# Kernel optimization log

Hardware: AMD Instinct MI355X
Metric: run time of the kernel (lower is better)

The kernel has to match this reference:

```python
import jax, jax.numpy as jnp
import numpy as np
from jax import lax

# Per-tensor power-of-two scales (ScalingImplType.CONST / POWER_OF_TWO in Brevitas)
S_ACT8 = 2.0 ** -4   # 8-bit signed input quant scale
S_ACT4 = 2.0 ** -1   # 4-bit signed input quant scale
S_W = 2.0 ** -2      # per-tensor weight quant scale
S_RELU = 2.0 ** -2   # 4-bit unsigned QuantReLU scale


def fq(x, scale, qmin, qmax):
    # fake-quant with straight-through estimator (STE)
    q = jnp.clip(jnp.round(x / scale), qmin, qmax) * scale
    return x + lax.stop_gradient(q - x)


def fq_signed(x, scale, bits):
    return fq(x, scale, -(2 ** (bits - 1)), 2 ** (bits - 1) - 1)


def fq_uint(x, scale, bits):
    return fq(x, scale, 0, 2 ** bits - 1)


def qconv(x, w, in_bits, w_bits, s_in, stride=1, padding=0, groups=1):
    xq = fq_signed(x, s_in, in_bits)
    wq = fq_signed(w, S_W, w_bits)
    return lax.conv_general_dilated(
        xq, wq, (stride, stride), [(padding, padding)] * 2,
        feature_group_count=groups,
        dimension_numbers=('NCHW', 'OIHW', 'NCHW'))


def maxpool(x, k, s):
    return lax.reduce_window(x, -jnp.inf, lax.max,
                             (1, 1, k, k), (1, 1, s, s), 'VALID')


def dwsep(x, dw, pw):
    c = x.shape[1]
    x = qconv(x, dw, 4, 4, S_ACT4, padding=1, groups=c)  # depthwise 3x3
    x = qconv(x, pw, 4, 4, S_ACT4)                       # pointwise 1x1
    return x


def qrelu4(x):
    return fq_uint(jax.nn.relu(x), S_RELU, 4)


def setup_inputs() -> dict:
    key = jax.random.key(0)
    ks = jax.random.split(key, 10)
    B = 1024
    mk = lambda k, shp, sc=0.5: jax.random.normal(k, shp, jnp.float32) * sc
    return {
        'x': jax.random.normal(ks[0], (B, 3, 32, 32), jnp.float32),
        'w0': mk(ks[1], (3, 3, 1, 1)),
        'dw1': mk(ks[2], (3, 1, 3, 3)),
        'pw1': mk(ks[3], (32, 3, 1, 1)),
        'dw2': mk(ks[4], (32, 1, 3, 3)),
        'pw2': mk(ks[5], (64, 32, 1, 1)),
        'dw3': mk(ks[6], (64, 1, 3, 3)),
        'pw3': mk(ks[7], (128, 64, 1, 1)),
        'wc1': mk(ks[8], (256, 128, 1, 1)),
        'wc2': mk(ks[9], (10, 256, 1, 1)),
    }


def reference(x, w0, dw1, pw1, dw2, pw2, dw3, pw3, wc1, wc2):
    # features
    h = qconv(x, w0, 8, 8, S_ACT8)            # 1x1, 3->3, 8-bit
    h = dwsep(h, dw1, pw1)                    # 3->32, 32x32
    h = qrelu4(h)
    h = maxpool(h, 2, 2)                      # 16x16
    h = dwsep(h, dw2, pw2)                    # 32->64
    h = qrelu4(h)
    h = maxpool(h, 2, 2)                      # 8x8
    h = dwsep(h, dw3, pw3)                    # 64->128
    h = qrelu4(h)
    h = maxpool(h, 8, 1)                      # 1x1
    # classifier
    h = qconv(h, wc1, 4, 4, S_ACT4)           # 128->256
    h = qrelu4(h)
    h = qconv(h, wc2, 4, 4, S_ACT4)           # 256->10
    h = fq_signed(h, S_ACT8, 8)               # output quant int8
    return h
```

## Files before the change

kernel.cpp:

```cpp
#include <hip/hip_runtime.h>

typedef int v4i __attribute__((ext_vector_type(4)));

#define W0i   0
#define DW1i  9
#define PW1i  36
#define DW2i  132
#define WC1p  3556
#define WC2p  11748
#define PW2Fb 12388
#define PW3Fb 12900
#define DW2pk 14948
#define DW3pk 15092
#define WTOT  15380

__device__ __attribute__((aligned(16))) int g_wsq[WTOT];

__device__ __forceinline__ int iclamp(int v, int lo, int hi) {
  return v < lo ? lo : (v > hi ? hi : v);
}
__device__ __forceinline__ int rne4(int a) {
  return (a + 1 + ((a >> 2) & 1)) >> 2;
}
__device__ __forceinline__ int rne32(int a) {
  return (a + 15 + ((a >> 5) & 1)) >> 5;
}

__device__ __forceinline__ void bar_lds() {
  asm volatile("s_waitcnt lgkmcnt(0)\n\ts_barrier" ::: "memory");
}

__device__ __forceinline__ int dot4(int a, int b, int c) {
#if defined(__has_builtin) && __has_builtin(__builtin_amdgcn_sdot4)
  return __builtin_amdgcn_sdot4(a, b, c, false);
#else
  c += ((a << 24) >> 24) * ((b << 24) >> 24);
  c += ((a << 16) >> 24) * ((b << 16) >> 24);
  c += ((a <<  8) >> 24) * ((b <<  8) >> 24);
  c += (a >> 24) * (b >> 24);
  return c;
#endif
}

__device__ __forceinline__ int alignb(int hi, int lo, int sh) {
#if defined(__has_builtin) && __has_builtin(__builtin_amdgcn_alignbyte)
  return __builtin_amdgcn_alignbyte(hi, lo, sh);
#else
  return (int)(((((unsigned long long)(unsigned)hi) << 32) |
                (unsigned)lo) >> (8 * sh));
#endif
}

__device__ __forceinline__ int pack3(int a, int b, int c) {
  return (a & 0xff) | ((b & 0xff) << 8) | ((c & 0xff) << 16);
}

__device__ __forceinline__ int pk_mad16(int a, int b, int c) {
  int d;
  asm("v_pk_mad_i16 %0, %1, %2, %3" : "=v"(d) : "v"(a), "v"(b), "v"(c));
  return d;
}
__device__ __forceinline__ int pk_add16(int a, int b) {
  int d;
  asm("v_pk_add_i16 %0, %1, %2" : "=v"(d) : "v"(a), "v"(b));
  return d;
}
__device__ __forceinline__ int pk_ashr16(int sh, int a) {
  int d;
  asm("v_pk_ashrrev_i16 %0, %1, %2" : "=v"(d) : "v"(sh), "v"(a));
  return d;
}
__device__ __forceinline__ int pk_max16(int a, int b) {
  int d;
  asm("v_pk_max_i16 %0, %1, %2" : "=v"(d) : "v"(a), "v"(b));
  return d;
}
__device__ __forceinline__ int pk_min16(int a, int b) {
  int d;
  asm("v_pk_min_i16 %0, %1, %2" : "=v"(d) : "v"(a), "v"(b));
  return d;
}
__device__ __forceinline__ int rne4s_pk(int a) {
  const int sh = 0x00020002, one = 0x00010001;
  int t = pk_ashr16(sh, a);
  t &= one;
  t += one;
  int s4 = pk_add16(a, t);
  int r = pk_ashr16(sh, s4);
  r = pk_max16(r, (int)0xFFF8FFF8);
  r = pk_min16(r, 0x00070007);
  return r;
}

__device__ __forceinline__ int max4(v4i d) {
  int a = d[0] > d[1] ? d[0] : d[1];
  int b = d[2] > d[3] ? d[2] : d[3];
  return a > b ? a : b;
}

__global__ __launch_bounds__(256) void prep_weights(
    const float* __restrict__ w0,  const float* __restrict__ dw1,
    const float* __restrict__ pw1, const float* __restrict__ dw2,
    const float* __restrict__ pw2, const float* __restrict__ dw3,
    const float* __restrict__ pw3, const float* __restrict__ wc1,
    const float* __restrict__ wc2) {
  int t = blockIdx.x * blockDim.x + threadIdx.x;
  if (t >= WTOT) return;
  if (t >= DW2i && t < WC1p) return;
  if (t < DW2i) {
    float w; int lo = -8, hi = 7;
    if (t < DW1i)      { w = w0[t];        lo = -128; hi = 127; }
    else if (t < PW1i)   w = dw1[t - DW1i];
    else                 w = pw1[t - PW1i];
    g_wsq[t] = iclamp((int)rintf(w * 4.f), lo, hi);
  } else if (t < PW2Fb) {
    const float* src = (t < WC2p) ? wc1 + (t - WC1p) * 4
                                  : wc2 + (t - WC2p) * 4;
    int p = 0;
#pragma unroll
    for (int b = 0; b < 4; b++) {
      int c = iclamp((int)rintf(src[b] * 4.f), -8, 7);
      p |= (c & 0xff) << (8 * b);
    }
    g_wsq[t] = p;
  } else if (t < DW2pk) {
    int i = t - PW2Fb;
    int nt = i >> 7, r = i & 127, lane = r >> 1, dw = r & 1;
    int n = nt * 16 + (lane & 15);
    int kb = (lane >> 4) * 8 + dw * 4;
    int p = 0;
#pragma unroll
    for (int b = 0; b < 4; b++) {
      int c = iclamp((int)rintf(pw2[n * 32 + kb + b] * 4.f), -8, 7);
      p |= (c & 0xff) << (8 * b);
    }
    g_wsq[t] = p;
  } else if (t < DW2pk + 144) {
    int i = t - DW2pk;
    int cq = i / 18, r = i - cq * 18, t9 = r >> 1, par = r & 1;
    int wl = iclamp((int)rintf(dw2[(cq * 4 + par) * 9 + t9] * 4.f), -8, 7);
    int wh = iclamp((int)rintf(dw2[(cq * 4 + 2 + par) * 9 + t9] * 4.f), -8, 7);
    g_wsq[t] = (wl & 0xFFFF) | (wh << 16);
  } else {
    int i = t - DW3pk;
    int cq = i / 18, r = i - cq * 18, t9 = r >> 1, par = r & 1;
    int wl = iclamp((int)rintf(dw3[(cq * 4 + par) * 9 + t9] * 4.f), -8, 7);
    int wh = iclamp((int)rintf(dw3[(cq * 4 + 2 + par) * 9 + t9] * 4.f), -8, 7);
    g_wsq[t] = (wl & 0xFFFF) | (wh << 16);
  }
}

__global__ __launch_bounds__(256) void prep_weights_pw3(
    const float* __restrict__ pw3) {
  int t = PW3Fb + blockIdx.x * blockDim.x + threadIdx.x;
  if (t >= DW2pk) return;
  int i = t - PW3Fb;
  int g = i >> 7, r = i & 127, lane = r >> 1, dw = r & 1;
  int nt = g >> 1, kh = g & 1;
  int n = nt * 16 + (lane & 15);
  int kb = kh * 32 + (lane >> 4) * 8 + dw * 4;
  int p = 0;
#pragma unroll
  for (int b = 0; b < 4; b++) {
    int c = iclamp((int)rintf(pw3[n * 64 + kb + b] * 4.f), -8, 7);
    p |= (c & 0xff) << (8 * b);
  }
  g_wsq[t] = p;
}

__global__ __launch_bounds__(256, 4) void fused_net(
    const float* __restrict__ x,
    float* __restrict__ out)
{
  const int img = blockIdx.x;
  const int tid = threadIdx.x;
  const int wv = tid >> 6, lane = tid & 63;
  const int lm = lane & 15, kg = lane >> 4;
  const int* __restrict__ wq = g_wsq;

  __shared__ __align__(16) int bufAi[2560];
  __shared__ __align__(16) int bufBi[2592];

  const int ntp = (wv & 1) * 2;
  const long bw0 = *(const long*)(wq + PW2Fb + (ntp * 64 + lane) * 2);
  const long bw1 = *(const long*)(wq + PW2Fb + ((ntp + 1) * 64 + lane) * 2);
  long b0v[2], b1v[2];
#pragma unroll
  for (int h = 0; h < 2; h++) {
    int nt = wv * 2 + h;
    b0v[h] = *(const long*)(wq + PW3Fb + (nt * 2 + 0) * 128 + lane * 2);
    b1v[h] = *(const long*)(wq + PW3Fb + (nt * 2 + 1) * 128 + lane * 2);
  }

  {
    const float* xim = x + (size_t)img * 3072;
    const int p4 = tid * 4;
    float4 v0 = *(const float4*)(xim + p4);
    float4 v1 = *(const float4*)(xim + 1024 + p4);
    float4 v2 = *(const float4*)(xim + 2048 + p4);
    int w[9];
#pragma unroll
    for (int i = 0; i < 9; i++) w[i] = wq[W0i + i];
#define Q8(v) iclamp((int)rintf((v) * 16.f), -128, 127)
    int a0[4] = {Q8(v0.x), Q8(v0.y), Q8(v0.z), Q8(v0.w)};
    int a1[4] = {Q8(v1.x), Q8(v1.y), Q8(v1.z), Q8(v1.w)};
    int a2[4] = {Q8(v2.x), Q8(v2.y), Q8(v2.z), Q8(v2.w)};
#undef Q8
#pragma unroll
    for (int o = 0; o < 3; o++) {
      int pk = 0;
#pragma unroll
      for (int j = 0; j < 4; j++) {
        int s = a0[j] * w[o * 3] + a1[j] * w[o * 3 + 1] + a2[j] * w[o * 3 + 2];
        pk |= (iclamp(rne32(s), -8, 7) & 0xff) << (8 * j);
      }
      bufAi[o * 256 + tid] = pk;
    }
  }
  bar_lds();

  {
    const int py = tid >> 4, px = tid & 15;
    int wr[3][3], wrh[3][3];
#pragma unroll
    for (int c = 0; c < 3; c++)
#pragma unroll
      for (int ky = 0; ky < 3; ky++) {
        int w = pack3(wq[DW1i + c * 9 + ky * 3],
                      wq[DW1i + c * 9 + ky * 3 + 1],
                      wq[DW1i + c * 9 + ky * 3 + 2]);
        wr[c][ky] = w;
        wrh[c][ky] = w << 8;
      }
    const int s = (px & 1) ? 1 : 3;
    const int D0 = (2 * px - 1) >> 2;
    int V[3][4];
#pragma unroll
    for (int r = 0; r < 4; r++) {
      int rr = 2 * py - 1 + r;
      bool ok = (unsigned)rr < 32u;
#pragma unroll
      for (int c = 0; c < 3; c++) {
        int lo = 0, hi = 0;
        if (ok) {
          const int* ap = bufAi + c * 256 + rr * 8;
          if (px > 0)  lo = ap[D0];
          if (px < 15) hi = ap[D0 + 1];
        }
        V[c][r] = alignb(hi, lo, s);
      }
    }
    int a[4];
#pragma unroll
    for (int dy = 0; dy < 2; dy++) {
      int r01[3];
#pragma unroll
      for (int c = 0; c < 3; c++) {
        int acc0 = 0, acc1 = 0;
#pragma unroll
        for (int ky = 0; ky < 3; ky++) {
          acc0 = dot4(V[c][dy + ky], wr[c][ky], acc0);
          acc1 = dot4(V[c][dy + ky], wrh[c][ky], acc1);
        }
        int p = (int)__builtin_amdgcn_perm((unsigned)acc1, (unsigned)acc0,
                                           0x05040100u);
        r01[c] = rne4s_pk(p);
      }
      unsigned t0 = __builtin_amdgcn_perm((unsigned)r01[1], (unsigned)r01[0],
                                          0x0C0C0400u);
      a[2 * dy] = (int)__builtin_amdgcn_perm((unsigned)r01[2], t0, 0x0C040100u);
      unsigned t1 = __builtin_amdgcn_perm((unsigned)r01[1], (unsigned)r01[0],
                                          0x0C0C0602u);
      a[2 * dy + 1] =
          (int)__builtin_amdgcn_perm((unsigned)r01[2], t1, 0x0C060100u);
    }
#pragma unroll
    for (int it = 0; it < 8; it++) {
      int pk = 0;
#pragma unroll
      for (int j = 0; j < 4; j++) {
        int o = it * 4 + j;
        int wpk = pack3(wq[PW1i + o * 3], wq[PW1i + o * 3 + 1],
                        wq[PW1i + o * 3 + 2]);
        int m0 = dot4(a[0], wpk, 0), m1 = dot4(a[1], wpk, 0);
        int m2 = dot4(a[2], wpk, 0), m3 = dot4(a[3], wpk, 0);
        int mx = max(max(m0, m1), max(m2, m3));
        pk |= iclamp(rne4(mx), 0, 7) << (8 * j);
      }
      bufBi[py * 149 + px * 9 + it] = pk;
    }
  }
  bar_lds();

  {
    const int cq = tid >> 5;
    const int rem = tid & 31;
    const int y = rem >> 1, xh = rem & 1, x0 = xh * 8;
    int we[9], wo[9];
    {
      const int2* wp = (const int2*)(wq + DW2pk + cq * 18);
#pragma unroll
      for (int t9 = 0; t9 < 9; t9++) { int2 v = wp[t9]; we[t9] = v.x; wo[t9] = v.y; }
    }
    int acce[8] = {}, acco[8] = {};
#pragma unroll
    for (int ky = 0; ky < 3; ky++) {
      int yy = y + ky - 1;
      if (yy < 0 || yy > 15) continue;
      int rb = yy * 149 + cq;
      int rd[10];
      rd[0] = (x0 > 0) ? bufBi[rb + (x0 - 1) * 9] : 0;
#pragma unroll
      for (int k = 1; k < 9; k++) rd[k] = bufBi[rb + (x0 - 1 + k) * 9];
      rd[9] = (x0 < 8) ? bufBi[rb + (x0 + 8) * 9] : 0;
      int ee[10], eo[10];
#pragma unroll
      for (int k = 0; k < 10; k++) {
        ee[k] = rd[k] & 0x000F000F;
        eo[k] = (rd[k] >> 8) & 0x000F000F;
      }
#pragma unroll
      for (int j = 0; j < 8; j++)
#pragma unroll
        for (int kx = 0; kx < 3; kx++) {
          acce[j] = pk_mad16(ee[j + kx], we[ky * 3 + kx], acce[j]);
          acco[j] = pk_mad16(eo[j + kx], wo[ky * 3 + kx], acco[j]);
        }
    }
    const int py = y >> 1, dy = y & 1;
#pragma unroll
    for (int j = 0; j < 8; j++) {
      int xx = x0 + j;
      int qp = py * 8 + (xx >> 1);
      int q = qp ^ (py & 3);
      int m = q * 4 + dy * 2 + (xx & 1);
      int re = rne4s_pk(acce[j]);
      int ro = rne4s_pk(acco[j]);
      bufAi[m * 10 + cq] = (re & 0x00FF00FF) | ((ro & 0x00FF00FF) << 8);
    }
  }
  bar_lds();

  {
    const int mtb = (wv >> 1) * 8;
    const signed char* Ab = (const signed char*)bufAi;
    signed char* A2c = (signed char*)bufBi;
    const int n0 = ntp * 16 + lm, n1 = (ntp + 1) * 16 + lm;
#pragma unroll 4
    for (int mt = mtb; mt < mtb + 8; mt++) {
      int m = mt * 16 + lm;
      long av = *(const long*)(Ab + m * 40 + kg * 8);
      v4i d0 = __builtin_amdgcn_mfma_i32_16x16x32_i8(av, bw0, (v4i){0, 0, 0, 0},
                                                     0, 0, 0);
      v4i d1 = __builtin_amdgcn_mfma_i32_16x16x32_i8(av, bw1, (v4i){0, 0, 0, 0},
                                                     0, 0, 0);
      int q = mt * 4 + kg;
      int qp = q ^ ((q >> 3) & 3);
      int py = qp >> 3, px = qp & 7;
      int bb = (py * 137 + px * 17) * 4;
      A2c[bb + n0] = (signed char)iclamp(rne4(max4(d0)), 0, 7);
      A2c[bb + n1] = (signed char)iclamp(rne4(max4(d1)), 0, 7);
    }
  }
  bar_lds();

  {
    int cq2 = tid >> 4;
    int s = tid & 15;
    int y = s >> 1, x0 = (s & 1) << 2;
    int we[9], wo[9];
    {
      const int2* wp = (const int2*)(wq + DW3pk + cq2 * 18);
#pragma unroll
      for (int t9 = 0; t9 < 9; t9++) { int2 v = wp[t9]; we[t9] = v.x; wo[t9] = v.y; }
    }
    int acce[4] = {}, acco[4] = {};
#pragma unroll
    for (int ky = 0; ky < 3; ky++) {
      int yy = y + ky - 1;
      if (yy < 0 || yy > 7) continue;
      int rb = yy * 137 + cq2;
      int rd[6];
      rd[0] = (x0 == 4) ? bufBi[rb + (x0 - 1) * 17] : 0;
      rd[1] = bufBi[rb + x0 * 17];
      rd[2] = bufBi[rb + (x0 + 1) * 17];
      rd[3] = bufBi[rb + (x0 + 2) * 17];
      rd[4] = bufBi[rb + (x0 + 3) * 17];
      rd[5] = (x0 == 0) ? bufBi[rb + (x0 + 4) * 17] : 0;
      int ee[6], eo[6];
#pragma unroll
      for (int k = 0; k < 6; k++) {
        ee[k] = rd[k] & 0x000F000F;
        eo[k] = (rd[k] >> 8) & 0x000F000F;
      }
#pragma unroll
      for (int j = 0; j < 4; j++)
#pragma unroll
        for (int kx = 0; kx < 3; kx++) {
          acce[j] = pk_mad16(ee[j + kx], we[ky * 3 + kx], acce[j]);
          acco[j] = pk_mad16(eo[j + kx], wo[ky * 3 + kx], acco[j]);
        }
    }
#pragma unroll
    for (int j = 0; j < 4; j++) {
      int re = rne4s_pk(acce[j]);
      int ro = rne4s_pk(acco[j]);
      bufAi[(y * 8 + x0 + j) * 18 + cq2] =
          (re & 0x00FF00FF) | ((ro & 0x00FF00FF) << 8);
    }
  }
  int4 wfc[8];
  {
    const int4* wp = (const int4*)(wq + WC1p + tid * 32);
#pragma unroll
    for (int rI = 0; rI < 8; rI++) wfc[rI] = wp[rI];
  }
  bar_lds();

  {
    const signed char* Ab = (const signed char*)bufAi;
    signed char* fcin = (signed char*)bufBi;
    int mx[2] = {-1000000, -1000000};
#pragma unroll
    for (int mt = 0; mt < 4; mt++) {
      int m = mt * 16 + lm;
      long a0 = *(const long*)(Ab + m * 72 + kg * 8);
      long a1 = *(const long*)(Ab + m * 72 + 32 + kg * 8);
#pragma unroll
      for (int h = 0; h < 2; h++) {
        v4i d = __builtin_amdgcn_mfma_i32_16x16x32_i8(a0, b0v[h],
                                                      (v4i){0, 0, 0, 0}, 0, 0, 0);
        d = __builtin_amdgcn_mfma_i32_16x16x32_i8(a1, b1v[h], d, 0, 0, 0);
        int t4 = max4(d);
        mx[h] = mx[h] > t4 ? mx[h] : t4;
      }
    }
#pragma unroll
    for (int h = 0; h < 2; h++) {
      int red = max(mx[h], __shfl_xor(mx[h], 16));
      red = max(red, __shfl_xor(red, 32));
      if (lane < 16)
        fcin[(wv * 2 + h) * 16 + lm] = (signed char)iclamp(rne4(red), 0, 7);
    }
  }
  bar_lds();

  {
    const int4* mp = (const int4*)bufBi;
    int acc = 0;
#pragma unroll
    for (int rI = 0; rI < 8; rI++) {
      int4 a = mp[rI]; int4 w = wfc[rI];
      acc = dot4(a.x, w.x, acc); acc = dot4(a.y, w.y, acc);
      acc = dot4(a.z, w.z, acc); acc = dot4(a.w, w.w, acc);
    }
    ((signed char*)bufAi)[tid] = (signed char)iclamp(rne4(acc), 0, 7);
  }
  bar_lds();

  if (tid < 40) {
    int k = tid >> 2, j = tid & 3;
    const int4* wp = (const int4*)(wq + WC2p + k * 64 + j * 16);
    const int4* ap = (const int4*)bufAi;
    int acc = 0;
#pragma unroll
    for (int r = 0; r < 4; r++) {
      int4 a = ap[j * 4 + r]; int4 w = wp[r];
      acc = dot4(a.x, w.x, acc); acc = dot4(a.y, w.y, acc);
      acc = dot4(a.z, w.z, acc); acc = dot4(a.w, w.w, acc);
    }
    acc += __shfl_xor(acc, 1);
    acc += __shfl_xor(acc, 2);
    if (j == 0) {
      int code = iclamp(2 * acc, -128, 127);
      out[(size_t)img * 10 + k] = (float)code * 0.0625f;
    }
  }
}

extern "C" void kernel_launch(void* const* d_in, const int* in_sizes, int n_in,
                              void* d_out, int out_size, void* d_ws, size_t ws_size,
                              hipStream_t stream) {
  (void)d_ws; (void)ws_size; (void)in_sizes; (void)n_in; (void)out_size;
  const float* x   = (const float*)d_in[0];
  const float* w0  = (const float*)d_in[1];
  const float* dw1 = (const float*)d_in[2];
  const float* pw1 = (const float*)d_in[3];
  const float* dw2 = (const float*)d_in[4];
  const float* pw2 = (const float*)d_in[5];
  const float* dw3 = (const float*)d_in[6];
  const float* pw3 = (const float*)d_in[7];
  const float* wc1 = (const float*)d_in[8];
  const float* wc2 = (const float*)d_in[9];
  float* out = (float*)d_out;

  prep_weights<<<(WTOT + 255) / 256, 256, 0, stream>>>(
      w0, dw1, pw1, dw2, pw2, dw3, pw3, wc1, wc2);
  prep_weights_pw3<<<(DW2pk - PW3Fb + 255) / 256, 256, 0, stream>>>(pw3);
  fused_net<<<1024, 256, 0, stream>>>(x, out);
}
```

Before: 98.83 us.

## Process two images per block and fold pw3 weight prep into main prep kernel

Each block now handles two images with doubled LDS buffers, amortizing per-block weight register loads and barrier overhead over twice the work; grid halves to 512 blocks and launch bounds drop to 2 blocks/CU. The pw1 pointwise weights are hoisted into 32 registers once, and the separate pw3 weight-prep kernel is merged into the main prep kernel, removing one launch. This risks lower occupancy and fewer blocks than CUs (512 blocks on a 256-CU device gives two per CU), plus higher register pressure.

Result: faster. 96.72 us (-2.1%).

```diff
diff --git a/kernel.cpp b/kernel.cpp
--- a/kernel.cpp
+++ b/kernel.cpp
@@ -123,7 +123,7 @@
       p |= (c & 0xff) << (8 * b);
     }
     g_wsq[t] = p;
-  } else if (t < DW2pk) {
+  } else if (t < PW3Fb) {
     int i = t - PW2Fb;
     int nt = i >> 7, r = i & 127, lane = r >> 1, dw = r & 1;
     int n = nt * 16 + (lane & 15);
@@ -135,7 +135,20 @@
       p |= (c & 0xff) << (8 * b);
     }
     g_wsq[t] = p;
-  } else if (t < DW2pk + 144) {
+  } else if (t < DW2pk) {
+    int i = t - PW3Fb;
+    int g = i >> 7, r = i & 127, lane = r >> 1, dw = r & 1;
+    int nt = g >> 1, kh = g & 1;
+    int n = nt * 16 + (lane & 15);
+    int kb = kh * 32 + (lane >> 4) * 8 + dw * 4;
+    int p = 0;
+#pragma unroll
+    for (int b = 0; b < 4; b++) {
+      int c = iclamp((int)rintf(pw3[n * 64 + kb + b] * 4.f), -8, 7);
+      p |= (c & 0xff) << (8 * b);
+    }
+    g_wsq[t] = p;
+  } else if (t < DW3pk) {
     int i = t - DW2pk;
     int cq = i / 18, r = i - cq * 18, t9 = r >> 1, par = r & 1;
     int wl = iclamp((int)rintf(dw2[(cq * 4 + par) * 9 + t9] * 4.f), -8, 7);
@@ -150,36 +163,18 @@
   }
 }
 
-__global__ __launch_bounds__(256) void prep_weights_pw3(
-    const float* __restrict__ pw3) {
-  int t = PW3Fb + blockIdx.x * blockDim.x + threadIdx.x;
-  if (t >= DW2pk) return;
-  int i = t - PW3Fb;
-  int g = i >> 7, r = i & 127, lane = r >> 1, dw = r & 1;
-  int nt = g >> 1, kh = g & 1;
-  int n = nt * 16 + (lane & 15);
-  int kb = kh * 32 + (lane >> 4) * 8 + dw * 4;
-  int p = 0;
-#pragma unroll
-  for (int b = 0; b < 4; b++) {
-    int c = iclamp((int)rintf(pw3[n * 64 + kb + b] * 4.f), -8, 7);
-    p |= (c & 0xff) << (8 * b);
-  }
-  g_wsq[t] = p;
-}
-
-__global__ __launch_bounds__(256, 4) void fused_net(
+__global__ __launch_bounds__(256, 2) void fused_net(
     const float* __restrict__ x,
     float* __restrict__ out)
 {
-  const int img = blockIdx.x;
+  const int img0 = blockIdx.x * 2;
   const int tid = threadIdx.x;
   const int wv = tid >> 6, lane = tid & 63;
   const int lm = lane & 15, kg = lane >> 4;
   const int* __restrict__ wq = g_wsq;
 
-  __shared__ __align__(16) int bufAi[2560];
-  __shared__ __align__(16) int bufBi[2592];
+  __shared__ __align__(16) int bufAi[2][2560];
+  __shared__ __align__(16) int bufBi[2][2592];
 
   const int ntp = (wv & 1) * 2;
   const long bw0 = *(const long*)(wq + PW2Fb + (ntp * 64 + lane) * 2);
@@ -193,29 +188,41 @@
   }
 
   {
-    const float* xim = x + (size_t)img * 3072;
     const int p4 = tid * 4;
-    float4 v0 = *(const float4*)(xim + p4);
-    float4 v1 = *(const float4*)(xim + 1024 + p4);
-    float4 v2 = *(const float4*)(xim + 2048 + p4);
+    float4 v[2][3];
+#pragma unroll
+    for (int ii = 0; ii < 2; ii++) {
+      const float* xim = x + (size_t)(img0 + ii) * 3072;
+      v[ii][0] = *(const float4*)(xim + p4);
+      v[ii][1] = *(const float4*)(xim + 1024 + p4);
+      v[ii][2] = *(const float4*)(xim + 2048 + p4);
+    }
     int w[9];
 #pragma unroll
     for (int i = 0; i < 9; i++) w[i] = wq[W0i + i];
-#define Q8(v) iclamp((int)rintf((v) * 16.f), -128, 127)
-    int a0[4] = {Q8(v0.x), Q8(v0.y), Q8(v0.z), Q8(v0.w)};
-    int a1[4] = {Q8(v1.x), Q8(v1.y), Q8(v1.z), Q8(v1.w)};
-    int a2[4] = {Q8(v2.x), Q8(v2.y), Q8(v2.z), Q8(v2.w)};
+#define Q8(vv) iclamp((int)rintf((vv) * 16.f), -128, 127)
+#pragma unroll
+    for (int ii = 0; ii < 2; ii++) {
+      int aq[3][4];
+#pragma unroll
+      for (int c = 0; c < 3; c++) {
+        float4 vv = v[ii][c];
+        aq[c][0] = Q8(vv.x); aq[c][1] = Q8(vv.y);
+        aq[c][2] = Q8(vv.z); aq[c][3] = Q8(vv.w);
+      }
+#pragma unroll
+      for (int o = 0; o < 3; o++) {
+        int pk = 0;
+#pragma unroll
+        for (int j = 0; j < 4; j++) {
+          int s = aq[0][j] * w[o * 3] + aq[1][j] * w[o * 3 + 1] +
+                  aq[2][j] * w[o * 3 + 2];
+          pk |= (iclamp(rne32(s), -8, 7) & 0xff) << (8 * j);
+        }
+        bufAi[ii][o * 256 + tid] = pk;
+      }
+    }
 #undef Q8
-#pragma unroll
-    for (int o = 0; o < 3; o++) {
-      int pk = 0;
-#pragma unroll
-      for (int j = 0; j < 4; j++) {
-        int s = a0[j] * w[o * 3] + a1[j] * w[o * 3 + 1] + a2[j] * w[o * 3 + 2];
-        pk |= (iclamp(rne32(s), -8, 7) & 0xff) << (8 * j);
-      }
-      bufAi[o * 256 + tid] = pk;
-    }
   }
   bar_lds();
 
@@ -232,62 +239,69 @@
         wr[c][ky] = w;
         wrh[c][ky] = w << 8;
       }
+    int wpw[32];
+#pragma unroll
+    for (int o = 0; o < 32; o++)
+      wpw[o] = pack3(wq[PW1i + o * 3], wq[PW1i + o * 3 + 1],
+                     wq[PW1i + o * 3 + 2]);
     const int s = (px & 1) ? 1 : 3;
     const int D0 = (2 * px - 1) >> 2;
-    int V[3][4];
-#pragma unroll
-    for (int r = 0; r < 4; r++) {
-      int rr = 2 * py - 1 + r;
-      bool ok = (unsigned)rr < 32u;
-#pragma unroll
-      for (int c = 0; c < 3; c++) {
-        int lo = 0, hi = 0;
-        if (ok) {
-          const int* ap = bufAi + c * 256 + rr * 8;
-          if (px > 0)  lo = ap[D0];
-          if (px < 15) hi = ap[D0 + 1];
-        }
-        V[c][r] = alignb(hi, lo, s);
-      }
-    }
-    int a[4];
-#pragma unroll
-    for (int dy = 0; dy < 2; dy++) {
-      int r01[3];
-#pragma unroll
-      for (int c = 0; c < 3; c++) {
-        int acc0 = 0, acc1 = 0;
-#pragma unroll
-        for (int ky = 0; ky < 3; ky++) {
-          acc0 = dot4(V[c][dy + ky], wr[c][ky], acc0);
-          acc1 = dot4(V[c][dy + ky], wrh[c][ky], acc1);
-        }
-        int p = (int)__builtin_amdgcn_perm((unsigned)acc1, (unsigned)acc0,
-                                           0x05040100u);
-        r01[c] = rne4s_pk(p);
-      }
-      unsigned t0 = __builtin_amdgcn_perm((unsigned)r01[1], (unsigned)r01[0],
-                                          0x0C0C0400u);
-      a[2 * dy] = (int)__builtin_amdgcn_perm((unsigned)r01[2], t0, 0x0C040100u);
-      unsigned t1 = __builtin_amdgcn_perm((unsigned)r01[1], (unsigned)r01[0],
-                                          0x0C0C0602u);
-      a[2 * dy + 1] =
-          (int)__builtin_amdgcn_perm((unsigned)r01[2], t1, 0x0C060100u);
-    }
-#pragma unroll
-    for (int it = 0; it < 8; it++) {
-      int pk = 0;
-#pragma unroll
-      for (int j = 0; j < 4; j++) {
-        int o = it * 4 + j;
-        int wpk = pack3(wq[PW1i + o * 3], wq[PW1i + o * 3 + 1],
-                        wq[PW1i + o * 3 + 2]);
-        int m0 = dot4(a[0], wpk, 0), m1 = dot4(a[1], wpk, 0);
-        int m2 = dot4(a[2], wpk, 0), m3 = dot4(a[3], wpk, 0);
-        int mx = max(max(m0, m1), max(m2, m3));
-        pk |= iclamp(rne4(mx), 0, 7) << (8 * j);
-      }
-      bufBi[py * 149 + px * 9 + it] = pk;
+#pragma unroll
+    for (int ii = 0; ii < 2; ii++) {
+      int V[3][4];
+#pragma unroll
+      for (int r = 0; r < 4; r++) {
+        int rr = 2 * py - 1 + r;
+        bool ok = (unsigned)rr < 32u;
+#pragma unroll
+        for (int c = 0; c < 3; c++) {
+          int lo = 0, hi = 0;
+          if (ok) {
+            const int* ap = &bufAi[ii][c * 256 + rr * 8];
+            if (px > 0)  lo = ap[D0];
+            if (px < 15) hi = ap[D0 + 1];
+          }
+          V[c][r] = alignb(hi, lo, s);
+        }
+      }
+      int a[4];
+#pragma unroll
+      for (int dy = 0; dy < 2; dy++) {
+        int r01[3];
+#pragma unroll
+        for (int c = 0; c < 3; c++) {
+          int acc0 = 0, acc1 = 0;
+#pragma unroll
+          for (int ky = 0; ky < 3; ky++) {
+            acc0 = dot4(V[c][dy + ky], wr[c][ky], acc0);
+            acc1 = dot4(V[c][dy + ky], wrh[c][ky], acc1);
+          }
+          int p = (int)__builtin_amdgcn_perm((unsigned)acc1, (unsigned)acc0,
+                                             0x05040100u);
+          r01[c] = rne4s_pk(p);
+        }
+        unsigned t0 = __builtin_amdgcn_perm((unsigned)r01[1], (unsigned)r01[0],
+                                            0x0C0C0400u);
+        a[2 * dy] =
+            (int)__builtin_amdgcn_perm((unsigned)r01[2], t0, 0x0C040100u);
+        unsigned t1 = __builtin_amdgcn_perm((unsigned)r01[1], (unsigned)r01[0],
+                                            0x0C0C0602u);
+        a[2 * dy + 1] =
+            (int)__builtin_amdgcn_perm((unsigned)r01[2], t1, 0x0C060100u);
+      }
+#pragma unroll
+      for (int it = 0; it < 8; it++) {
+        int pk = 0;
+#pragma unroll
+        for (int j = 0; j < 4; j++) {
+          int wpk = wpw[it * 4 + j];
+          int m0 = dot4(a[0], wpk, 0), m1 = dot4(a[1], wpk, 0);
+          int m2 = dot4(a[2], wpk, 0), m3 = dot4(a[3], wpk, 0);
+          int mx = max(max(m0, m1), max(m2, m3));
+          pk |= iclamp(rne4(mx), 0, 7) << (8 * j);
+        }
+        bufBi[ii][py * 149 + px * 9 + it] = pk;
+      }
     }
   }
   bar_lds();
@@ -302,64 +316,70 @@
 #pragma unroll
       for (int t9 = 0; t9 < 9; t9++) { int2 v = wp[t9]; we[t9] = v.x; wo[t9] = v.y; }
     }
-    int acce[8] = {}, acco[8] = {};
-#pragma unroll
-    for (int ky = 0; ky < 3; ky++) {
-      int yy = y + ky - 1;
-      if (yy < 0 || yy > 15) continue;
-      int rb = yy * 149 + cq;
-      int rd[10];
-      rd[0] = (x0 > 0) ? bufBi[rb + (x0 - 1) * 9] : 0;
-#pragma unroll
-      for (int k = 1; k < 9; k++) rd[k] = bufBi[rb + (x0 - 1 + k) * 9];
-      rd[9] = (x0 < 8) ? bufBi[rb + (x0 + 8) * 9] : 0;
-      int ee[10], eo[10];
-#pragma unroll
-      for (int k = 0; k < 10; k++) {
-        ee[k] = rd[k] & 0x000F000F;
-        eo[k] = (rd[k] >> 8) & 0x000F000F;
-      }
-#pragma unroll
-      for (int j = 0; j < 8; j++)
-#pragma unroll
-        for (int kx = 0; kx < 3; kx++) {
-          acce[j] = pk_mad16(ee[j + kx], we[ky * 3 + kx], acce[j]);
-          acco[j] = pk_mad16(eo[j + kx], wo[ky * 3 + kx], acco[j]);
-        }
-    }
     const int py = y >> 1, dy = y & 1;
 #pragma unroll
-    for (int j = 0; j < 8; j++) {
-      int xx = x0 + j;
-      int qp = py * 8 + (xx >> 1);
-      int q = qp ^ (py & 3);
-      int m = q * 4 + dy * 2 + (xx & 1);
-      int re = rne4s_pk(acce[j]);
-      int ro = rne4s_pk(acco[j]);
-      bufAi[m * 10 + cq] = (re & 0x00FF00FF) | ((ro & 0x00FF00FF) << 8);
+    for (int ii = 0; ii < 2; ii++) {
+      int acce[8] = {}, acco[8] = {};
+#pragma unroll
+      for (int ky = 0; ky < 3; ky++) {
+        int yy = y + ky - 1;
+        if (yy < 0 || yy > 15) continue;
+        int rb = yy * 149 + cq;
+        int rd[10];
+        rd[0] = (x0 > 0) ? bufBi[ii][rb + (x0 - 1) * 9] : 0;
+#pragma unroll
+        for (int k = 1; k < 9; k++) rd[k] = bufBi[ii][rb + (x0 - 1 + k) * 9];
+        rd[9] = (x0 < 8) ? bufBi[ii][rb + (x0 + 8) * 9] : 0;
+        int ee[10], eo[10];
+#pragma unroll
+        for (int k = 0; k < 10; k++) {
+          ee[k] = rd[k] & 0x000F000F;
+          eo[k] = (rd[k] >> 8) & 0x000F000F;
+        }
+#pragma unroll
+        for (int j = 0; j < 8; j++)
+#pragma unroll
+          for (int kx = 0; kx < 3; kx++) {
+            acce[j] = pk_mad16(ee[j + kx], we[ky * 3 + kx], acce[j]);
+            acco[j] = pk_mad16(eo[j + kx], wo[ky * 3 + kx], acco[j]);
+          }
+      }
+#pragma unroll
+      for (int j = 0; j < 8; j++) {
+        int xx = x0 + j;
+        int qp = py * 8 + (xx >> 1);
+        int q = qp ^ (py & 3);
+        int m = q * 4 + dy * 2 + (xx & 1);
+        int re = rne4s_pk(acce[j]);
+        int ro = rne4s_pk(acco[j]);
+        bufAi[ii][m * 10 + cq] = (re & 0x00FF00FF) | ((ro & 0x00FF00FF) << 8);
+      }
     }
   }
   bar_lds();
 
   {
     const int mtb = (wv >> 1) * 8;
-    const signed char* Ab = (const signed char*)bufAi;
-    signed char* A2c = (signed char*)bufBi;
     const int n0 = ntp * 16 + lm, n1 = (ntp + 1) * 16 + lm;
+#pragma unroll
+    for (int ii = 0; ii < 2; ii++) {
+      const signed char* Ab = (const signed char*)bufAi[ii];
+      signed char* A2c = (signed char*)bufBi[ii];
 #pragma unroll 4
-    for (int mt = mtb; mt < mtb + 8; mt++) {
-      int m = mt * 16 + lm;
-      long av = *(const long*)(Ab + m * 40 + kg * 8);
-      v4i d0 = __builtin_amdgcn_mfma_i32_16x16x32_i8(av, bw0, (v4i){0, 0, 0, 0},
-                                                     0, 0, 0);
-      v4i d1 = __builtin_amdgcn_mfma_i32_16x16x32_i8(av, bw1, (v4i){0, 0, 0, 0},
-                                                     0, 0, 0);
-      int q = mt * 4 + kg;
-      int qp = q ^ ((q >> 3) & 3);
-      int py = qp >> 3, px = qp & 7;
-      int bb = (py * 137 + px * 17) * 4;
-      A2c[bb + n0] = (signed char)iclamp(rne4(max4(d0)), 0, 7);
-      A2c[bb + n1] = (signed char)iclamp(rne4(max4(d1)), 0, 7);
+      for (int mt = mtb; mt < mtb + 8; mt++) {
+        int m = mt * 16 + lm;
+        long av = *(const long*)(Ab + m * 40 + kg * 8);
+        v4i d0 = __builtin_amdgcn_mfma_i32_16x16x32_i8(av, bw0,
+                                                       (v4i){0, 0, 0, 0}, 0, 0, 0);
+        v4i d1 = __builtin_amdgcn_mfma_i32_16x16x32_i8(av, bw1,
+                                                       (v4i){0, 0, 0, 0}, 0, 0, 0);
+        int q = mt * 4 + kg;
+        int qp = q ^ ((q >> 3) & 3);
+        int py = qp >> 3, px = qp & 7;
+        int bb = (py * 137 + px * 17) * 4;
+        A2c[bb + n0] = (signed char)iclamp(rne4(max4(d0)), 0, 7);
+        A2c[bb + n1] = (signed char)iclamp(rne4(max4(d1)), 0, 7);
+      }
     }
   }
   bar_lds();
@@ -374,39 +394,42 @@
 #pragma unroll
       for (int t9 = 0; t9 < 9; t9++) { int2 v = wp[t9]; we[t9] = v.x; wo[t9] = v.y; }
     }
-    int acce[4] = {}, acco[4] = {};
-#pragma unroll
-    for (int ky = 0; ky < 3; ky++) {
-      int yy = y + ky - 1;
-      if (yy < 0 || yy > 7) continue;
-      int rb = yy * 137 + cq2;
-      int rd[6];
-      rd[0] = (x0 == 4) ? bufBi[rb + (x0 - 1) * 17] : 0;
-      rd[1] = bufBi[rb + x0 * 17];
-      rd[2] = bufBi[rb + (x0 + 1) * 17];
-      rd[3] = bufBi[rb + (x0 + 2) * 17];
-      rd[4] = bufBi[rb + (x0 + 3) * 17];
-      rd[5] = (x0 == 0) ? bufBi[rb + (x0 + 4) * 17] : 0;
-      int ee[6], eo[6];
-#pragma unroll
-      for (int k = 0; k < 6; k++) {
-        ee[k] = rd[k] & 0x000F000F;
-        eo[k] = (rd[k] >> 8) & 0x000F000F;
-      }
-#pragma unroll
-      for (int j = 0; j < 4; j++)
-#pragma unroll
-        for (int kx = 0; kx < 3; kx++) {
-          acce[j] = pk_mad16(ee[j + kx], we[ky * 3 + kx], acce[j]);
-          acco[j] = pk_mad16(eo[j + kx], wo[ky * 3 + kx], acco[j]);
-        }
-    }
-#pragma unroll
-    for (int j = 0; j < 4; j++) {
-      int re = rne4s_pk(acce[j]);
-      int ro = rne4s_pk(acco[j]);
-      bufAi[(y * 8 + x0 + j) * 18 + cq2] =
-          (re & 0x00FF00FF) | ((ro & 0x00FF00FF) << 8);
+#pragma unroll
+    for (int ii = 0; ii < 2; ii++) {
+      int acce[4] = {}, acco[4] = {};
+#pragma unroll
+      for (int ky = 0; ky < 3; ky++) {
+        int yy = y + ky - 1;
+        if (yy < 0 || yy > 7) continue;
+        int rb = yy * 137 + cq2;
+        int rd[6];
+        rd[0] = (x0 == 4) ? bufBi[ii][rb + (x0 - 1) * 17] : 0;
+        rd[1] = bufBi[ii][rb + x0 * 17];
+        rd[2] = bufBi[ii][rb + (x0 + 1) * 17];
+        rd[3] = bufBi[ii][rb + (x0 + 2) * 17];
+        rd[4] = bufBi[ii][rb + (x0 + 3) * 17];
+        rd[5] = (x0 == 0) ? bufBi[ii][rb + (x0 + 4) * 17] : 0;
+        int ee[6], eo[6];
+#pragma unroll
+        for (int k = 0; k < 6; k++) {
+          ee[k] = rd[k] & 0x000F000F;
+          eo[k] = (rd[k] >> 8) & 0x000F000F;
+        }
+#pragma unroll
+        for (int j = 0; j < 4; j++)
+#pragma unroll
+          for (int kx = 0; kx < 3; kx++) {
+            acce[j] = pk_mad16(ee[j + kx], we[ky * 3 + kx], acce[j]);
+            acco[j] = pk_mad16(eo[j + kx], wo[ky * 3 + kx], acco[j]);
+          }
+      }
+#pragma unroll
+      for (int j = 0; j < 4; j++) {
+        int re = rne4s_pk(acce[j]);
+        int ro = rne4s_pk(acco[j]);
+        bufAi[ii][(y * 8 + x0 + j) * 18 + cq2] =
+            (re & 0x00FF00FF) | ((ro & 0x00FF00FF) << 8);
+      }
     }
   }
   int4 wfc[8];
@@ -418,62 +441,72 @@
   bar_lds();
 
   {
-    const signed char* Ab = (const signed char*)bufAi;
-    signed char* fcin = (signed char*)bufBi;
-    int mx[2] = {-1000000, -1000000};
-#pragma unroll
-    for (int mt = 0; mt < 4; mt++) {
-      int m = mt * 16 + lm;
-      long a0 = *(const long*)(Ab + m * 72 + kg * 8);
-      long a1 = *(const long*)(Ab + m * 72 + 32 + kg * 8);
+#pragma unroll
+    for (int ii = 0; ii < 2; ii++) {
+      const signed char* Ab = (const signed char*)bufAi[ii];
+      signed char* fcin = (signed char*)bufBi[ii];
+      int mx[2] = {-1000000, -1000000};
+#pragma unroll
+      for (int mt = 0; mt < 4; mt++) {
+        int m = mt * 16 + lm;
+        long a0 = *(const long*)(Ab + m * 72 + kg * 8);
+        long a1 = *(const long*)(Ab + m * 72 + 32 + kg * 8);
+#pragma unroll
+        for (int h = 0; h < 2; h++) {
+          v4i d = __builtin_amdgcn_mfma_i32_16x16x32_i8(a0, b0v[h],
+                                                        (v4i){0, 0, 0, 0}, 0, 0, 0);
+          d = __builtin_amdgcn_mfma_i32_16x16x32_i8(a1, b1v[h], d, 0, 0, 0);
+          int t4 = max4(d);
+          mx[h] = mx[h] > t4 ? mx[h] : t4;
+        }
+      }
 #pragma unroll
       for (int h = 0; h < 2; h++) {
-        v4i d = __builtin_amdgcn_mfma_i32_16x16x32_i8(a0, b0v[h],
-                                                      (v4i){0, 0, 0, 0}, 0, 0, 0);
-        d = __builtin_amdgcn_mfma_i32_16x16x32_i8(a1, b1v[h], d, 0, 0, 0);
-        int t4 = max4(d);
-        mx[h] = mx[h] > t4 ? mx[h] : t4;
-      }
-    }
-#pragma unroll
-    for (int h = 0; h < 2; h++) {
-      int red = max(mx[h], __shfl_xor(mx[h], 16));
-      red = max(red, __shfl_xor(red, 32));
-      if (lane < 16)
-        fcin[(wv * 2 + h) * 16 + lm] = (signed char)iclamp(rne4(red), 0, 7);
-    }
-  }
-  bar_lds();
-
-  {
-    const int4* mp = (const int4*)bufBi;
-    int acc = 0;
-#pragma unroll
-    for (int rI = 0; rI < 8; rI++) {
-      int4 a = mp[rI]; int4 w = wfc[rI];
-      acc = dot4(a.x, w.x, acc); acc = dot4(a.y, w.y, acc);
-      acc = dot4(a.z, w.z, acc); acc = dot4(a.w, w.w, acc);
-    }
-    ((signed char*)bufAi)[tid] = (signed char)iclamp(rne4(acc), 0, 7);
-  }
-  bar_lds();
-
-  if (tid < 40) {
-    int k = tid >> 2, j = tid & 3;
-    const int4* wp = (const int4*)(wq + WC2p + k * 64 + j * 16);
-    const int4* ap = (const int4*)bufAi;
-    int acc = 0;
-#pragma unroll
-    for (int r = 0; r < 4; r++) {
-      int4 a = ap[j * 4 + r]; int4 w = wp[r];
-      acc = dot4(a.x, w.x, acc); acc = dot4(a.y, w.y, acc);
-      acc = dot4(a.z, w.z, acc); acc = dot4(a.w, w.w, acc);
-    }
-    acc += __shfl_xor(acc, 1);
-    acc += __shfl_xor(acc, 2);
-    if (j == 0) {
-      int code = iclamp(2 * acc, -128, 127);
-      out[(size_t)img * 10 + k] = (float)code * 0.0625f;
+        int red = max(mx[h], __shfl_xor(mx[h], 16));
+        red = max(red, __shfl_xor(red, 32));
+        if (lane < 16)
+          fcin[(wv * 2 + h) * 16 + lm] = (signed char)iclamp(rne4(red), 0, 7);
+      }
+    }
+  }
+  bar_lds();
+
+  {
+#pragma unroll
+    for (int ii = 0; ii < 2; ii++) {
+      const int4* mp = (const int4*)bufBi[ii];
+      int acc = 0;
+#pragma unroll
+      for (int rI = 0; rI < 8; rI++) {
+        int4 a = mp[rI]; int4 w = wfc[rI];
+        acc = dot4(a.x, w.x, acc); acc = dot4(a.y, w.y, acc);
+        acc = dot4(a.z, w.z, acc); acc = dot4(a.w, w.w, acc);
+      }
+      ((signed char*)bufAi[ii])[tid] = (signed char)iclamp(rne4(acc), 0, 7);
+    }
+  }
+  bar_lds();
+
+  {
+    const int half = tid >> 7;
+    const int t = tid & 127;
+    if (t < 40) {
+      int k = t >> 2, j = t & 3;
+      const int4* wp = (const int4*)(wq + WC2p + k * 64 + j * 16);
+      const int4* ap = (const int4*)bufAi[half];
+      int acc = 0;
+#pragma unroll
+      for (int r = 0; r < 4; r++) {
+        int4 a = ap[j * 4 + r]; int4 w = wp[r];
+        acc = dot4(a.x, w.x, acc); acc = dot4(a.y, w.y, acc);
+        acc = dot4(a.z, w.z, acc); acc = dot4(a.w, w.w, acc);
+      }
+      acc += __shfl_xor(acc, 1);
+      acc += __shfl_xor(acc, 2);
+      if (j == 0) {
+        int code = iclamp(2 * acc, -128, 127);
+        out[(size_t)(img0 + half) * 10 + k] = (float)code * 0.0625f;
+      }
     }
   }
 }
@@ -496,6 +529,5 @@
 
   prep_weights<<<(WTOT + 255) / 256, 256, 0, stream>>>(
       w0, dw1, pw1, dw2, pw2, dw3, pw3, wc1, wc2);
-  prep_weights_pw3<<<(DW2pk - PW3Fb + 255) / 256, 256, 0, stream>>>(pw3);
-  fused_net<<<1024, 256, 0, stream>>>(x, out);
-}
+  fused_net<<<512, 256, 0, stream>>>(x, out);
+}
```

## Double fused_net block to 512 threads and merge weight prep into one kernel

Applied to the files above, without the earlier changes.

Each per-image block now runs 512 threads, and every stage is repartitioned so each thread does half the work. This covers the pointwise-1 channel halves, the dw2/dw3 columns, the pw2 m-tiles, the pw3 n-tiles and a split-K FC1 with a shuffle reduction. The pw3 weight prep is folded into the single prep kernel, and pw1/dw1 weights are prepacked to skip per-thread pack3 work. The goal is more parallelism per image and one fewer launch, at the cost of higher register-pressure limits and some stages (the input conv) leaving half the threads idle.

After: 93.45 us. 1.06x faster.

```diff
diff --git a/kernel.cpp b/kernel.cpp
--- a/kernel.cpp
+++ b/kernel.cpp
@@ -6,6 +6,8 @@
 #define DW1i  9
 #define PW1i  36
 #define DW2i  132
+#define PW1pk 132
+#define DW1pk 164
 #define WC1p  3556
 #define WC2p  11748
 #define PW2Fb 12388
@@ -54,6 +56,9 @@
 __device__ __forceinline__ int pack3(int a, int b, int c) {
   return (a & 0xff) | ((b & 0xff) << 8) | ((c & 0xff) << 16);
 }
+__device__ __forceinline__ int q4w(float w) {
+  return iclamp((int)rintf(w * 4.f), -8, 7);
+}
 
 __device__ __forceinline__ int pk_mad16(int a, int b, int c) {
   int d;
@@ -106,13 +111,20 @@
     const float* __restrict__ wc2) {
   int t = blockIdx.x * blockDim.x + threadIdx.x;
   if (t >= WTOT) return;
-  if (t >= DW2i && t < WC1p) return;
   if (t < DW2i) {
     float w; int lo = -8, hi = 7;
     if (t < DW1i)      { w = w0[t];        lo = -128; hi = 127; }
     else if (t < PW1i)   w = dw1[t - DW1i];
     else                 w = pw1[t - PW1i];
     g_wsq[t] = iclamp((int)rintf(w * 4.f), lo, hi);
+  } else if (t < PW1pk + 32) {
+    int o = t - PW1pk;
+    g_wsq[t] = pack3(q4w(pw1[3 * o]), q4w(pw1[3 * o + 1]), q4w(pw1[3 * o + 2]));
+  } else if (t < DW1pk + 9) {
+    int i = t - DW1pk;
+    g_wsq[t] = pack3(q4w(dw1[3 * i]), q4w(dw1[3 * i + 1]), q4w(dw1[3 * i + 2]));
+  } else if (t < WC1p) {
+    return;
   } else if (t < PW2Fb) {
     const float* src = (t < WC2p) ? wc1 + (t - WC1p) * 4
                                   : wc2 + (t - WC2p) * 4;
@@ -123,7 +135,7 @@
       p |= (c & 0xff) << (8 * b);
     }
     g_wsq[t] = p;
-  } else if (t < DW2pk) {
+  } else if (t < PW3Fb) {
     int i = t - PW2Fb;
     int nt = i >> 7, r = i & 127, lane = r >> 1, dw = r & 1;
     int n = nt * 16 + (lane & 15);
@@ -135,40 +147,35 @@
       p |= (c & 0xff) << (8 * b);
     }
     g_wsq[t] = p;
-  } else if (t < DW2pk + 144) {
+  } else if (t < DW2pk) {
+    int i = t - PW3Fb;
+    int g = i >> 7, r = i & 127, lane = r >> 1, dw = r & 1;
+    int nt = g >> 1, kh = g & 1;
+    int n = nt * 16 + (lane & 15);
+    int kb = kh * 32 + (lane >> 4) * 8 + dw * 4;
+    int p = 0;
+#pragma unroll
+    for (int b = 0; b < 4; b++) {
+      int c = iclamp((int)rintf(pw3[n * 64 + kb + b] * 4.f), -8, 7);
+      p |= (c & 0xff) << (8 * b);
+    }
+    g_wsq[t] = p;
+  } else if (t < DW3pk) {
     int i = t - DW2pk;
     int cq = i / 18, r = i - cq * 18, t9 = r >> 1, par = r & 1;
-    int wl = iclamp((int)rintf(dw2[(cq * 4 + par) * 9 + t9] * 4.f), -8, 7);
-    int wh = iclamp((int)rintf(dw2[(cq * 4 + 2 + par) * 9 + t9] * 4.f), -8, 7);
+    int wl = q4w(dw2[(cq * 4 + par) * 9 + t9]);
+    int wh = q4w(dw2[(cq * 4 + 2 + par) * 9 + t9]);
     g_wsq[t] = (wl & 0xFFFF) | (wh << 16);
   } else {
     int i = t - DW3pk;
     int cq = i / 18, r = i - cq * 18, t9 = r >> 1, par = r & 1;
-    int wl = iclamp((int)rintf(dw3[(cq * 4 + par) * 9 + t9] * 4.f), -8, 7);
-    int wh = iclamp((int)rintf(dw3[(cq * 4 + 2 + par) * 9 + t9] * 4.f), -8, 7);
+    int wl = q4w(dw3[(cq * 4 + par) * 9 + t9]);
+    int wh = q4w(dw3[(cq * 4 + 2 + par) * 9 + t9]);
     g_wsq[t] = (wl & 0xFFFF) | (wh << 16);
   }
 }
 
-__global__ __launch_bounds__(256) void prep_weights_pw3(
-    const float* __restrict__ pw3) {
-  int t = PW3Fb + blockIdx.x * blockDim.x + threadIdx.x;
-  if (t >= DW2pk) return;
-  int i = t - PW3Fb;
-  int g = i >> 7, r = i & 127, lane = r >> 1, dw = r & 1;
-  int nt = g >> 1, kh = g & 1;
-  int n = nt * 16 + (lane & 15);
-  int kb = kh * 32 + (lane >> 4) * 8 + dw * 4;
-  int p = 0;
-#pragma unroll
-  for (int b = 0; b < 4; b++) {
-    int c = iclamp((int)rintf(pw3[n * 64 + kb + b] * 4.f), -8, 7);
-    p |= (c & 0xff) << (8 * b);
-  }
-  g_wsq[t] = p;
-}
-
-__global__ __launch_bounds__(256, 4) void fused_net(
+__global__ __launch_bounds__(512, 8) void fused_net(
     const float* __restrict__ x,
     float* __restrict__ out)
 {
@@ -184,15 +191,10 @@
   const int ntp = (wv & 1) * 2;
   const long bw0 = *(const long*)(wq + PW2Fb + (ntp * 64 + lane) * 2);
   const long bw1 = *(const long*)(wq + PW2Fb + ((ntp + 1) * 64 + lane) * 2);
-  long b0v[2], b1v[2];
-#pragma unroll
-  for (int h = 0; h < 2; h++) {
-    int nt = wv * 2 + h;
-    b0v[h] = *(const long*)(wq + PW3Fb + (nt * 2 + 0) * 128 + lane * 2);
-    b1v[h] = *(const long*)(wq + PW3Fb + (nt * 2 + 1) * 128 + lane * 2);
-  }
-
-  {
+  const long b0v = *(const long*)(wq + PW3Fb + (wv * 2 + 0) * 128 + lane * 2);
+  const long b1v = *(const long*)(wq + PW3Fb + (wv * 2 + 1) * 128 + lane * 2);
+
+  if (tid < 256) {
     const float* xim = x + (size_t)img * 3072;
     const int p4 = tid * 4;
     float4 v0 = *(const float4*)(xim + p4);
@@ -220,15 +222,14 @@
   bar_lds();
 
   {
-    const int py = tid >> 4, px = tid & 15;
+    const int pos = tid & 255, half = tid >> 8;
+    const int py = pos >> 4, px = pos & 15;
     int wr[3][3], wrh[3][3];
 #pragma unroll
     for (int c = 0; c < 3; c++)
 #pragma unroll
       for (int ky = 0; ky < 3; ky++) {
-        int w = pack3(wq[DW1i + c * 9 + ky * 3],
-                      wq[DW1i + c * 9 + ky * 3 + 1],
-                      wq[DW1i + c * 9 + ky * 3 + 2]);
+        int w = wq[DW1pk + c * 3 + ky];
         wr[c][ky] = w;
         wrh[c][ky] = w << 8;
       }
@@ -275,13 +276,12 @@
           (int)__builtin_amdgcn_perm((unsigned)r01[2], t1, 0x0C060100u);
     }
 #pragma unroll
-    for (int it = 0; it < 8; it++) {
+    for (int it2 = 0; it2 < 4; it2++) {
+      int it = half * 4 + it2;
       int pk = 0;
 #pragma unroll
       for (int j = 0; j < 4; j++) {
-        int o = it * 4 + j;
-        int wpk = pack3(wq[PW1i + o * 3], wq[PW1i + o * 3 + 1],
-                        wq[PW1i + o * 3 + 2]);
+        int wpk = wq[PW1pk + it * 4 + j];
         int m0 = dot4(a[0], wpk, 0), m1 = dot4(a[1], wpk, 0);
         int m2 = dot4(a[2], wpk, 0), m3 = dot4(a[3], wpk, 0);
         int mx = max(max(m0, m1), max(m2, m3));
@@ -293,34 +293,34 @@
   bar_lds();
 
   {
-    const int cq = tid >> 5;
-    const int rem = tid & 31;
-    const int y = rem >> 1, xh = rem & 1, x0 = xh * 8;
+    const int cq = tid >> 6;
+    const int rem = tid & 63;
+    const int y = rem >> 2, xq = rem & 3, x0 = xq * 4;
     int we[9], wo[9];
     {
       const int2* wp = (const int2*)(wq + DW2pk + cq * 18);
 #pragma unroll
       for (int t9 = 0; t9 < 9; t9++) { int2 v = wp[t9]; we[t9] = v.x; wo[t9] = v.y; }
     }
-    int acce[8] = {}, acco[8] = {};
+    int acce[4] = {}, acco[4] = {};
 #pragma unroll
     for (int ky = 0; ky < 3; ky++) {
       int yy = y + ky - 1;
       if (yy < 0 || yy > 15) continue;
       int rb = yy * 149 + cq;
-      int rd[10];
+      int rd[6];
       rd[0] = (x0 > 0) ? bufBi[rb + (x0 - 1) * 9] : 0;
 #pragma unroll
-      for (int k = 1; k < 9; k++) rd[k] = bufBi[rb + (x0 - 1 + k) * 9];
-      rd[9] = (x0 < 8) ? bufBi[rb + (x0 + 8) * 9] : 0;
-      int ee[10], eo[10];
-#pragma unroll
-      for (int k = 0; k < 10; k++) {
+      for (int k = 1; k < 5; k++) rd[k] = bufBi[rb + (x0 - 1 + k) * 9];
+      rd[5] = (x0 < 12) ? bufBi[rb + (x0 + 4) * 9] : 0;
+      int ee[6], eo[6];
+#pragma unroll
+      for (int k = 0; k < 6; k++) {
         ee[k] = rd[k] & 0x000F000F;
         eo[k] = (rd[k] >> 8) & 0x000F000F;
       }
 #pragma unroll
-      for (int j = 0; j < 8; j++)
+      for (int j = 0; j < 4; j++)
 #pragma unroll
         for (int kx = 0; kx < 3; kx++) {
           acce[j] = pk_mad16(ee[j + kx], we[ky * 3 + kx], acce[j]);
@@ -329,7 +329,7 @@
     }
     const int py = y >> 1, dy = y & 1;
 #pragma unroll
-    for (int j = 0; j < 8; j++) {
+    for (int j = 0; j < 4; j++) {
       int xx = x0 + j;
       int qp = py * 8 + (xx >> 1);
       int q = qp ^ (py & 3);
@@ -342,12 +342,12 @@
   bar_lds();
 
   {
-    const int mtb = (wv >> 1) * 8;
+    const int mtb = (wv >> 1) * 4;
     const signed char* Ab = (const signed char*)bufAi;
     signed char* A2c = (signed char*)bufBi;
     const int n0 = ntp * 16 + lm, n1 = (ntp + 1) * 16 + lm;
-#pragma unroll 4
-    for (int mt = mtb; mt < mtb + 8; mt++) {
+#pragma unroll
+    for (int mt = mtb; mt < mtb + 4; mt++) {
       int m = mt * 16 + lm;
       long av = *(const long*)(Ab + m * 40 + kg * 8);
       v4i d0 = __builtin_amdgcn_mfma_i32_16x16x32_i8(av, bw0, (v4i){0, 0, 0, 0},
@@ -365,36 +365,34 @@
   bar_lds();
 
   {
-    int cq2 = tid >> 4;
-    int s = tid & 15;
-    int y = s >> 1, x0 = (s & 1) << 2;
+    int cq2 = tid >> 5;
+    int s = tid & 31;
+    int y = s >> 2, x0 = (s & 3) << 1;
     int we[9], wo[9];
     {
       const int2* wp = (const int2*)(wq + DW3pk + cq2 * 18);
 #pragma unroll
       for (int t9 = 0; t9 < 9; t9++) { int2 v = wp[t9]; we[t9] = v.x; wo[t9] = v.y; }
     }
-    int acce[4] = {}, acco[4] = {};
+    int acce[2] = {}, acco[2] = {};
 #pragma unroll
     for (int ky = 0; ky < 3; ky++) {
       int yy = y + ky - 1;
       if (yy < 0 || yy > 7) continue;
       int rb = yy * 137 + cq2;
-      int rd[6];
-      rd[0] = (x0 == 4) ? bufBi[rb + (x0 - 1) * 17] : 0;
+      int rd[4];
+      rd[0] = (x0 > 0) ? bufBi[rb + (x0 - 1) * 17] : 0;
       rd[1] = bufBi[rb + x0 * 17];
       rd[2] = bufBi[rb + (x0 + 1) * 17];
-      rd[3] = bufBi[rb + (x0 + 2) * 17];
-      rd[4] = bufBi[rb + (x0 + 3) * 17];
-      rd[5] = (x0 == 0) ? bufBi[rb + (x0 + 4) * 17] : 0;
-      int ee[6], eo[6];
-#pragma unroll
-      for (int k = 0; k < 6; k++) {
+      rd[3] = (x0 < 6) ? bufBi[rb + (x0 + 2) * 17] : 0;
+      int ee[4], eo[4];
+#pragma unroll
+      for (int k = 0; k < 4; k++) {
         ee[k] = rd[k] & 0x000F000F;
         eo[k] = (rd[k] >> 8) & 0x000F000F;
       }
 #pragma unroll
-      for (int j = 0; j < 4; j++)
+      for (int j = 0; j < 2; j++)
 #pragma unroll
         for (int kx = 0; kx < 3; kx++) {
           acce[j] = pk_mad16(ee[j + kx], we[ky * 3 + kx], acce[j]);
@@ -402,59 +400,57 @@
         }
     }
 #pragma unroll
-    for (int j = 0; j < 4; j++) {
+    for (int j = 0; j < 2; j++) {
       int re = rne4s_pk(acce[j]);
       int ro = rne4s_pk(acco[j]);
       bufAi[(y * 8 + x0 + j) * 18 + cq2] =
           (re & 0x00FF00FF) | ((ro & 0x00FF00FF) << 8);
     }
   }
-  int4 wfc[8];
-  {
-    const int4* wp = (const int4*)(wq + WC1p + tid * 32);
-#pragma unroll
-    for (int rI = 0; rI < 8; rI++) wfc[rI] = wp[rI];
+  int4 wfc[4];
+  {
+    const int o = tid >> 1, sub = tid & 1;
+    const int4* wp = (const int4*)(wq + WC1p + o * 32 + sub * 16);
+#pragma unroll
+    for (int rI = 0; rI < 4; rI++) wfc[rI] = wp[rI];
   }
   bar_lds();
 
   {
     const signed char* Ab = (const signed char*)bufAi;
     signed char* fcin = (signed char*)bufBi;
-    int mx[2] = {-1000000, -1000000};
+    int mx = -1000000;
 #pragma unroll
     for (int mt = 0; mt < 4; mt++) {
       int m = mt * 16 + lm;
       long a0 = *(const long*)(Ab + m * 72 + kg * 8);
       long a1 = *(const long*)(Ab + m * 72 + 32 + kg * 8);
-#pragma unroll
-      for (int h = 0; h < 2; h++) {
-        v4i d = __builtin_amdgcn_mfma_i32_16x16x32_i8(a0, b0v[h],
-                                                      (v4i){0, 0, 0, 0}, 0, 0, 0);
-        d = __builtin_amdgcn_mfma_i32_16x16x32_i8(a1, b1v[h], d, 0, 0, 0);
-        int t4 = max4(d);
-        mx[h] = mx[h] > t4 ? mx[h] : t4;
-      }
-    }
-#pragma unroll
-    for (int h = 0; h < 2; h++) {
-      int red = max(mx[h], __shfl_xor(mx[h], 16));
-      red = max(red, __shfl_xor(red, 32));
-      if (lane < 16)
-        fcin[(wv * 2 + h) * 16 + lm] = (signed char)iclamp(rne4(red), 0, 7);
-    }
-  }
-  bar_lds();
-
-  {
-    const int4* mp = (const int4*)bufBi;
+      v4i d = __builtin_amdgcn_mfma_i32_16x16x32_i8(a0, b0v,
+                                                    (v4i){0, 0, 0, 0}, 0, 0, 0);
+      d = __builtin_amdgcn_mfma_i32_16x16x32_i8(a1, b1v, d, 0, 0, 0);
+      int t4 = max4(d);
+      mx = mx > t4 ? mx : t4;
+    }
+    int red = max(mx, __shfl_xor(mx, 16));
+    red = max(red, __shfl_xor(red, 32));
+    if (lane < 16)
+      fcin[wv * 16 + lm] = (signed char)iclamp(rne4(red), 0, 7);
+  }
+  bar_lds();
+
+  {
+    const int o = tid >> 1, sub = tid & 1;
+    const int4* mp = (const int4*)bufBi + sub * 4;
     int acc = 0;
 #pragma unroll
-    for (int rI = 0; rI < 8; rI++) {
+    for (int rI = 0; rI < 4; rI++) {
       int4 a = mp[rI]; int4 w = wfc[rI];
       acc = dot4(a.x, w.x, acc); acc = dot4(a.y, w.y, acc);
       acc = dot4(a.z, w.z, acc); acc = dot4(a.w, w.w, acc);
     }
-    ((signed char*)bufAi)[tid] = (signed char)iclamp(rne4(acc), 0, 7);
+    acc += __shfl_xor(acc, 1);
+    if (sub == 0)
+      ((signed char*)bufAi)[o] = (signed char)iclamp(rne4(acc), 0, 7);
   }
   bar_lds();
 
@@ -496,6 +492,5 @@
 
   prep_weights<<<(WTOT + 255) / 256, 256, 0, stream>>>(
       w0, dw1, pw1, dw2, pw2, dw3, pw3, wc1, wc2);
-  prep_weights_pw3<<<(DW2pk - PW3Fb + 255) / 256, 256, 0, stream>>>(pw3);
-  fused_net<<<1024, 256, 0, stream>>>(x, out);
-}
+  fused_net<<<1024, 512, 0, stream>>>(x, out);
+}
```
